# Kernel tuning notes

Measured on AMD Instinct MI355X. Metric: run time of the kernel, lower is better.

The kernel has to match this reference:

```python
import jax, jax.numpy as jnp
import numpy as np

B, T, C, L = 256, 512, 256, 64
NEG = -1e30  # log-space 'zero'
BLANK = 0


def setup_inputs() -> dict:
    key = jax.random.key(0)
    k1, k2, k3, k4 = jax.random.split(key, 4)
    logits = jax.random.normal(k1, (B, T, C), dtype=jnp.float32)
    targets = jax.random.randint(k2, (B, L), 1, C)            # labels never equal blank (0)
    input_lengths = jax.random.randint(k3, (B,), T - 100, T + 1)
    target_lengths = jax.random.randint(k4, (B,), L // 2, L + 1)
    return dict(logits=logits, targets=targets,
                input_lengths=input_lengths, target_lengths=target_lengths)


def _ctc_loss(logits, targets, input_lengths, target_lengths):
    Bb, Tt, Cc = logits.shape
    Ll = targets.shape[1]
    S = 2 * Ll + 1  # extended label length (blanks interleaved)

    # fused log_softmax over vocab (original does permute then log_softmax; same math)
    logp = jax.nn.log_softmax(logits, axis=-1)  # [B,T,C]

    # extended target sequence: blank, y1, blank, y2, ..., blank
    ext = jnp.zeros((Bb, S), jnp.int32).at[:, 1::2].set(targets.astype(jnp.int32))
    # gather log-probs of extended labels for every timestep: [B,T,S]
    lp_ext = jnp.take_along_axis(logp, jnp.broadcast_to(ext[:, None, :], (Bb, Tt, S)), axis=2)

    # skip transition s-2 -> s allowed iff ext[s] != blank and ext[s] != ext[s-2]
    skip = jnp.zeros((Bb, S), bool).at[:, 2:].set(
        (ext[:, 2:] != BLANK) & (ext[:, 2:] != ext[:, :-2]))

    # alpha at t=0
    alpha0 = (jnp.full((Bb, S), NEG, dtype=logits.dtype)
              .at[:, 0].set(lp_ext[:, 0, 0])
              .at[:, 1].set(lp_ext[:, 0, 1]))

    neg1 = jnp.full((Bb, 1), NEG, dtype=logits.dtype)
    neg2 = jnp.full((Bb, 2), NEG, dtype=logits.dtype)

    def step(alpha, inputs):
        lp_t, t = inputs  # lp_t: [B,S]
        a1 = alpha
        a2 = jnp.concatenate([neg1, alpha[:, :-1]], axis=1)
        a3 = jnp.where(skip, jnp.concatenate([neg2, alpha[:, :-2]], axis=1), NEG)
        new = jnp.logaddexp(jnp.logaddexp(a1, a2), a3) + lp_t
        new = jnp.maximum(new, NEG)  # keep impossible paths bounded
        # freeze alpha for batch rows whose input sequence already ended
        alpha = jnp.where((t < input_lengths)[:, None], new, alpha)
        return alpha, None

    ts = jnp.arange(1, Tt)
    alphaT, _ = jax.lax.scan(step, alpha0, (jnp.swapaxes(lp_ext, 0, 1)[1:], ts))

    tl = target_lengths.astype(jnp.int32)
    a_last = jnp.take_along_axis(alphaT, (2 * tl)[:, None], axis=1)[:, 0]
    a_prev = jnp.take_along_axis(alphaT, (2 * tl - 1)[:, None], axis=1)[:, 0]
    loss = -jnp.logaddexp(a_last, a_prev)            # [B]
    loss = jnp.where(loss > 1e20, 0.0, loss)          # zero_infinity=True
    # reduction='mean': per-sample loss divided by target length, then batch mean
    return (loss / tl.astype(loss.dtype)).mean()


def reference(logits, targets, input_lengths, target_lengths):
    return _ctc_loss(logits, targets, input_lengths, target_lengths)
```

## Files before the change

### kernel.cpp

```cpp
#include <hip/hip_runtime.h>

#define B_ 256
#define T_ 512
#define C_ 256
#define L_ 64
#define S_ 129
#define TCH 64
#define LOG2E 1.44269504f
#define LN2 0.69314718f

template <int CTRL>
__device__ __forceinline__ int dpp_mov_i32(int x) {
    return __builtin_amdgcn_update_dpp(0, x, CTRL, 0xF, 0xF, true);
}

__device__ __forceinline__ double shr1d(double x) {
    int2 u = __builtin_bit_cast(int2, x);
    u.x = dpp_mov_i32<0x138>(u.x);
    u.y = dpp_mov_i32<0x138>(u.y);
    return __builtin_bit_cast(double, u);
}

template <int CTRL>
__device__ __forceinline__ double dpp_mov_f64(double x) {
    int2 u = __builtin_bit_cast(int2, x);
    u.x = dpp_mov_i32<CTRL>(u.x);
    u.y = dpp_mov_i32<CTRL>(u.y);
    return __builtin_bit_cast(double, u);
}

__device__ __forceinline__ float wave_sum(float x) {
#define DPPADD(ctrl)                                                          \
    x += __builtin_bit_cast(float, dpp_mov_i32<ctrl>(__builtin_bit_cast(int, x)));
    DPPADD(0x111) DPPADD(0x112) DPPADD(0x114)
    DPPADD(0x118) DPPADD(0x142) DPPADD(0x143)
#undef DPPADD
    return __builtin_bit_cast(float,
        __builtin_amdgcn_readlane(__builtin_bit_cast(int, x), 63));
}

__device__ __forceinline__ double wave_max_d(double x) {
    x = fmax(x, dpp_mov_f64<0x111>(x));
    x = fmax(x, dpp_mov_f64<0x112>(x));
    x = fmax(x, dpp_mov_f64<0x114>(x));
    x = fmax(x, dpp_mov_f64<0x118>(x));
    x = fmax(x, dpp_mov_f64<0x142>(x));
    x = fmax(x, dpp_mov_f64<0x143>(x));
    int2 u = __builtin_bit_cast(int2, x);
    u.x = __builtin_amdgcn_readlane(u.x, 63);
    u.y = __builtin_amdgcn_readlane(u.y, 63);
    return __builtin_bit_cast(double, u);
}

__device__ __forceinline__ void rescale(double& a0, double& a1, double& a2, int& e) {
    const double m = wave_max_d(fmax(fmax(a0, a1), a2));
    const int hi = __builtin_bit_cast(int2, m).y;
    int ex = ((hi >> 20) & 0x7ff) - 1023;
    if (m == 0.0) ex = 0;
    e += ex;
    int2 fb; fb.x = 0; fb.y = (1023 - ex) << 20;
    const double f = __builtin_bit_cast(double, fb);
    a0 *= f; a1 *= f; a2 *= f;
}

__device__ __forceinline__ float log2_pos(double a) {
    if (a == 0.0) return -1e30f;
    int2 u = __builtin_bit_cast(int2, a);
    const int ex = ((u.y >> 20) & 0x7ff) - 1023;
    u.y = (u.y & 0x800FFFFF) | (1023 << 20);
    const float mf = (float)__builtin_bit_cast(double, u);
    return __log2f(mf) + (float)ex;
}

__global__ __launch_bounds__(576) void k_fused(const float* __restrict__ logits,
                                               const int* __restrict__ targets,
                                               const int* __restrict__ in_len,
                                               const int* __restrict__ tg_len,
                                               float* __restrict__ out) {
    const int b = blockIdx.x;
    const int w = threadIdx.x >> 6;
    const int l = threadIdx.x & 63;

    __shared__ float2 P[2][TCH][64];
    __shared__ float4 rb4[8][2][64];
    __shared__ int   tgt_sh[L_];
    __shared__ float alpha_sh[S_];

    if (threadIdx.x < L_) tgt_sh[threadIdx.x] = targets[(b << 6) + threadIdx.x];
    __syncthreads();

    const int len = in_len[b];
    double a0 = 0.0, a1 = 0.0, a2 = 0.0;
    int scale_total = 0;
    bool skip = false;
    if (w == 0) {
        const int tc = tgt_sh[l];
        const int tp = __shfl_up(tc, 1);
        skip = (l >= 1) && (tc != tp);
        __builtin_amdgcn_s_setprio(1);
    }
    const int mytgt = tgt_sh[l];

    const size_t rowbase = (size_t)b * T_;

    float4 va[8];
    if (w > 0) {
        const int tt0 = (w - 1) * 8;
        #pragma unroll
        for (int r = 0; r < 8; ++r)
            va[r] = ((const float4*)logits)[(rowbase + tt0 + r) * 64 + l];
    }

    for (int k = 0; k < 9; ++k) {
        if (w > 0 && k < 8) {
            const int tt0 = (w - 1) * 8;
            float4 vb[8];
            if (k < 7) {
                #pragma unroll
                for (int r = 0; r < 8; ++r) {
                    const int t = (k + 1) * TCH + tt0 + r;
                    vb[r] = ((const float4*)logits)[(rowbase + t) * 64 + l];
                }
            }
            #pragma unroll
            for (int r = 0; r < 8; ++r) {
                const int tt = tt0 + r;
                float4 e;
                e.x = exp2f(va[r].x * LOG2E);
                e.y = exp2f(va[r].y * LOG2E);
                e.z = exp2f(va[r].z * LOG2E);
                e.w = exp2f(va[r].w * LOG2E);
                rb4[w - 1][r & 1][l] = e;
                const float stot = wave_sum(e.x + e.y + e.z + e.w);
                const float rs = __builtin_amdgcn_rcpf(stot);
                const float eb = __builtin_bit_cast(float,
                    __builtin_amdgcn_readfirstlane(__builtin_bit_cast(int, e.x)));
                const float eo = ((const float*)&rb4[w - 1][r & 1][0])[mytgt];
                float2 pq; pq.x = eb * rs; pq.y = eo * rs;
                P[k & 1][tt][l] = pq;
            }
            #pragma unroll
            for (int r = 0; r < 8; ++r) va[r] = vb[r];
        }
        if (w == 0 && k >= 1) {
            const int kb = (k - 1) & 1;
            const int base = (k - 1) * TCH;
            float2 pa[8], pn[8];
            #pragma unroll
            for (int j = 0; j < 8; ++j) pa[j] = P[kb][j][l];
            if (base == 0) {
                a0 = (l == 0) ? (double)pa[0].x : 0.0;
                a1 = (l == 0) ? (double)pa[0].y : 0.0;
                a2 = 0.0;
            }
            for (int g = 0; g < 8; ++g) {
                if (g < 7) {
                    #pragma unroll
                    for (int j = 0; j < 8; ++j) pn[j] = P[kb][(g + 1) * 8 + j][l];
                }
                #pragma unroll
                for (int j = 0; j < 8; ++j) {
                    const int t = base + g * 8 + j;
                    if (t >= 1 && t < len) {
                        const double p = shr1d(a1);
                        const double c = skip ? p : 0.0;
                        const double a0n = (a0 + p) * (double)pa[j].x;
                        const double a1n = ((a1 + a0) + c) * (double)pa[j].y;
                        const double a2n = (a2 + a1) * (double)pa[j].x;
                        a0 = a0n; a1 = a1n; a2 = a2n;
                    }
                }
                if (g == 3 || g == 7) rescale(a0, a1, a2, scale_total);
                if (g < 7) {
                    #pragma unroll
                    for (int j = 0; j < 8; ++j) pa[j] = pn[j];
                }
            }
        }
        __syncthreads();
    }

    if (w == 0) {
        alpha_sh[2 * l]     = log2_pos(a0);
        alpha_sh[2 * l + 1] = log2_pos(a1);
        if (l == 63) alpha_sh[128] = log2_pos(a2);
    }
    __syncthreads();
    if (threadIdx.x == 0) {
        const int tl = tg_len[b];
        const float al = alpha_sh[2 * tl];
        const float ap = alpha_sh[2 * tl - 1];
        const float m  = fmaxf(al, ap);
        const float lse2 = m + __log2f(exp2f(al - m) + exp2f(ap - m));
        float loss = -LN2 * (lse2 + (float)scale_total);
        if (!(loss < 1e20f)) loss = 0.0f;
        atomicAdd(out, loss / (float)tl * (1.0f / (float)B_));
    }
}

extern "C" void kernel_launch(void* const* d_in, const int* in_sizes, int n_in,
                              void* d_out, int out_size, void* d_ws, size_t ws_size,
                              hipStream_t stream) {
    const float* logits  = (const float*)d_in[0];
    const int*   targets = (const int*)d_in[1];
    const int*   in_len  = (const int*)d_in[2];
    const int*   tg_len  = (const int*)d_in[3];
    float*       out     = (float*)d_out;

    (void)hipMemsetAsync(d_out, 0, sizeof(float), stream);
    k_fused<<<B_, 576, 0, stream>>>(logits, targets, in_len, tg_len, out);
}
```

Measured before the change: 203.5 us.

## Replace block barriers with LDS flag-based producer/consumer handoff between waves

Replaces the per-chunk __syncthreads lockstep between the eight producer waves (softmax and gather into P) and the single consumer wave (alpha recurrence) with workgroup-scope atomic counters. Producers spin until the consumer has freed a buffer slot, and the consumer spins until all eight producers have finished a chunk. Producers now return early instead of waiting at barriers. This lets producers run ahead and removes barrier stalls, at the cost of spin-waiting that competes for issue slots. It also relies on a single wave reading alpha_sh right after writing it without a barrier.

```diff
diff --git a/kernel.cpp b/kernel.cpp
--- a/kernel.cpp
+++ b/kernel.cpp
@@ -85,42 +85,35 @@
     __shared__ float4 rb4[8][2][64];
     __shared__ int   tgt_sh[L_];
     __shared__ float alpha_sh[S_];
-
+    __shared__ int   prod_done;
+    __shared__ int   cons_done;
+
+    if (threadIdx.x == 0) { prod_done = 0; cons_done = 0; }
     if (threadIdx.x < L_) tgt_sh[threadIdx.x] = targets[(b << 6) + threadIdx.x];
     __syncthreads();
 
     const int len = in_len[b];
-    double a0 = 0.0, a1 = 0.0, a2 = 0.0;
-    int scale_total = 0;
-    bool skip = false;
-    if (w == 0) {
-        const int tc = tgt_sh[l];
-        const int tp = __shfl_up(tc, 1);
-        skip = (l >= 1) && (tc != tp);
-        __builtin_amdgcn_s_setprio(1);
-    }
-    const int mytgt = tgt_sh[l];
-
     const size_t rowbase = (size_t)b * T_;
 
-    float4 va[8];
     if (w > 0) {
+        const int mytgt = tgt_sh[l];
         const int tt0 = (w - 1) * 8;
+        float4 va[8], vb[8];
         #pragma unroll
         for (int r = 0; r < 8; ++r)
             va[r] = ((const float4*)logits)[(rowbase + tt0 + r) * 64 + l];
-    }
-
-    for (int k = 0; k < 9; ++k) {
-        if (w > 0 && k < 8) {
-            const int tt0 = (w - 1) * 8;
-            float4 vb[8];
+
+        for (int k = 0; k < 8; ++k) {
             if (k < 7) {
                 #pragma unroll
                 for (int r = 0; r < 8; ++r) {
                     const int t = (k + 1) * TCH + tt0 + r;
                     vb[r] = ((const float4*)logits)[(rowbase + t) * 64 + l];
                 }
+            }
+            if (k >= 2) {
+                while (__hip_atomic_load(&cons_done, __ATOMIC_ACQUIRE,
+                                         __HIP_MEMORY_SCOPE_WORKGROUP) < k - 1) {}
             }
             #pragma unroll
             for (int r = 0; r < 8; ++r) {
@@ -139,55 +132,69 @@
                 float2 pq; pq.x = eb * rs; pq.y = eo * rs;
                 P[k & 1][tt][l] = pq;
             }
+            if (l == 0)
+                __hip_atomic_fetch_add(&prod_done, 1, __ATOMIC_RELEASE,
+                                       __HIP_MEMORY_SCOPE_WORKGROUP);
             #pragma unroll
             for (int r = 0; r < 8; ++r) va[r] = vb[r];
         }
-        if (w == 0 && k >= 1) {
-            const int kb = (k - 1) & 1;
-            const int base = (k - 1) * TCH;
-            float2 pa[8], pn[8];
+        return;
+    }
+
+    __builtin_amdgcn_s_setprio(1);
+    const int tc = tgt_sh[l];
+    const int tp = __shfl_up(tc, 1);
+    const bool skip = (l >= 1) && (tc != tp);
+    const int tl = tg_len[b];
+
+    double a0 = 0.0, a1 = 0.0, a2 = 0.0;
+    int scale_total = 0;
+
+    for (int k = 0; k < 8; ++k) {
+        while (__hip_atomic_load(&prod_done, __ATOMIC_ACQUIRE,
+                                 __HIP_MEMORY_SCOPE_WORKGROUP) < 8 * (k + 1)) {}
+        const int kb = k & 1;
+        const int base = k * TCH;
+        float2 pa[8], pn[8];
+        #pragma unroll
+        for (int j = 0; j < 8; ++j) pa[j] = P[kb][j][l];
+        if (k == 0) {
+            a0 = (l == 0) ? (double)pa[0].x : 0.0;
+            a1 = (l == 0) ? (double)pa[0].y : 0.0;
+            a2 = 0.0;
+        }
+        for (int g = 0; g < 8; ++g) {
+            if (g < 7) {
+                #pragma unroll
+                for (int j = 0; j < 8; ++j) pn[j] = P[kb][(g + 1) * 8 + j][l];
+            }
             #pragma unroll
-            for (int j = 0; j < 8; ++j) pa[j] = P[kb][j][l];
-            if (base == 0) {
-                a0 = (l == 0) ? (double)pa[0].x : 0.0;
-                a1 = (l == 0) ? (double)pa[0].y : 0.0;
-                a2 = 0.0;
-            }
-            for (int g = 0; g < 8; ++g) {
-                if (g < 7) {
-                    #pragma unroll
-                    for (int j = 0; j < 8; ++j) pn[j] = P[kb][(g + 1) * 8 + j][l];
+            for (int j = 0; j < 8; ++j) {
+                const int t = base + g * 8 + j;
+                if (t >= 1 && t < len) {
+                    const double p = shr1d(a1);
+                    const double c = skip ? p : 0.0;
+                    const double a0n = (a0 + p) * (double)pa[j].x;
+                    const double a1n = ((a1 + a0) + c) * (double)pa[j].y;
+                    const double a2n = (a2 + a1) * (double)pa[j].x;
+                    a0 = a0n; a1 = a1n; a2 = a2n;
                 }
+            }
+            if (g == 3 || g == 7) rescale(a0, a1, a2, scale_total);
+            if (g < 7) {
                 #pragma unroll
-                for (int j = 0; j < 8; ++j) {
-                    const int t = base + g * 8 + j;
-                    if (t >= 1 && t < len) {
-                        const double p = shr1d(a1);
-                        const double c = skip ? p : 0.0;
-                        const double a0n = (a0 + p) * (double)pa[j].x;
-                        const double a1n = ((a1 + a0) + c) * (double)pa[j].y;
-                        const double a2n = (a2 + a1) * (double)pa[j].x;
-                        a0 = a0n; a1 = a1n; a2 = a2n;
-                    }
-                }
-                if (g == 3 || g == 7) rescale(a0, a1, a2, scale_total);
-                if (g < 7) {
-                    #pragma unroll
-                    for (int j = 0; j < 8; ++j) pa[j] = pn[j];
-                }
+                for (int j = 0; j < 8; ++j) pa[j] = pn[j];
             }
         }
-        __syncthreads();
+        if (l == 0)
+            __hip_atomic_fetch_add(&cons_done, 1, __ATOMIC_RELEASE,
+                                   __HIP_MEMORY_SCOPE_WORKGROUP);
     }
 
-    if (w == 0) {
-        alpha_sh[2 * l]     = log2_pos(a0);
-        alpha_sh[2 * l + 1] = log2_pos(a1);
-        if (l == 63) alpha_sh[128] = log2_pos(a2);
-    }
-    __syncthreads();
-    if (threadIdx.x == 0) {
-        const int tl = tg_len[b];
+    alpha_sh[2 * l]     = log2_pos(a0);
+    alpha_sh[2 * l + 1] = log2_pos(a1);
+    if (l == 63) alpha_sh[128] = log2_pos(a2);
+    if (l == 0) {
         const float al = alpha_sh[2 * tl];
         const float ap = alpha_sh[2 * tl - 1];
         const float m  = fmaxf(al, ap);
```

Result: no change. 203.3 us (-0.1%).
